# Kernel tuning notes

Hardware: AMD Instinct MI355X
Metric: run time of the kernel (lower is better)

Reference implementation:

```python
import jax, jax.numpy as jnp
import numpy as np

B, T, D, H, C = 32, 512, 768, 512, 7


def setup_inputs() -> dict:
    key = jax.random.key(0)
    ks = jax.random.split(key, 10)
    g = lambda k, shape: jax.random.normal(k, shape, jnp.float32) * 0.02
    return {
        "x": jax.random.normal(ks[0], (B, T, D), jnp.float32),
        # PyTorch LSTM params; b = b_ih + b_hh folded into one bias (same math)
        "Wf_ih": g(ks[1], (4 * H, 2 * D)),
        "Wf_hh": g(ks[2], (4 * H, H)),
        "bf": jnp.zeros((4 * H,), jnp.float32),
        "Wb_ih": g(ks[3], (4 * H, 2 * D)),
        "Wb_hh": g(ks[4], (4 * H, H)),
        "bb": jnp.zeros((4 * H,), jnp.float32),
        "W_enc": g(ks[5], (H, D)),
        "b_enc": jnp.zeros((H,), jnp.float32),
        "W_dec": g(ks[6], (H, H)),
        "b_dec": jnp.zeros((H,), jnp.float32),
        "v": jax.random.uniform(ks[7], (H,), jnpp := jnp.float32) if False else jax.random.uniform(ks[7], (H,), jnp.float32),
        "W_head": g(ks[8], (C, 2 * H)),
        "b_head": jnp.zeros((C,), jnp.float32),
    }


def reference(x, Wf_ih, Wf_hh, bf, Wb_ih, Wb_hh, bb, W_enc, b_enc, W_dec, b_dec, v, W_head, b_head):
    hid = W_dec.shape[0]
    # encoder projection is time-invariant -> hoist out of the loop (same math as original)
    enc_proj = jnp.einsum('btd,hd->bth', x, W_enc) + b_enc  # (B,T,H)

    def run_direction(x_seq, Wih, Whh, b):
        def step(carry, xt):
            h, c = carry                                    # (B,H) each
            dec = h @ W_dec.T + b_dec                       # (B,H)
            scores = jnp.tanh(enc_proj + dec[:, None, :]) @ v  # (B,T)
            w = jax.nn.softmax(scores, axis=1)
            ctx = jnp.einsum('bt,btd->bd', w, x)            # (B,D)
            inp = jnp.concatenate([ctx, xt], axis=1)        # (B,2D)
            gates = inp @ Wih.T + h @ Whh.T + b             # (B,4H), torch order i,f,g,o
            i_, f_, g_, o_ = jnp.split(gates, 4, axis=1)
            c = jax.nn.sigmoid(f_) * c + jax.nn.sigmoid(i_) * jnp.tanh(g_)
            h = jax.nn.sigmoid(o_) * jnp.tanh(c)
            return (h, c), h

        h0 = jnp.zeros((x.shape[0], hid), x.dtype)
        (_, _), hs = jax.lax.scan(step, (h0, h0), x_seq)
        return hs                                           # (T,B,H)

    x_seq = jnp.swapaxes(x, 0, 1)                           # (T,B,D)
    hs_f = run_direction(x_seq, Wf_ih, Wf_hh, bf)
    hs_b = run_direction(x_seq[::-1], Wb_ih, Wb_hh, bb)[::-1]
    comb = jnp.swapaxes(jnp.concatenate([hs_f, hs_b], axis=-1), 0, 1)  # (B,T,2H)
    return comb @ W_head.T + b_head                          # (B,T,C)
```

## Files before the change

### kernel.cpp

```cpp
#include <hip/hip_runtime.h>
#include <cstdint>
#include <cstddef>

#define L2E 1.4426950408889634f

typedef __attribute__((ext_vector_type(8))) short short8v;
typedef __attribute__((ext_vector_type(4))) float f32x4;
typedef unsigned long long ull;

__device__ __forceinline__ float fexp2(float x){ return __builtin_amdgcn_exp2f(x); }
__device__ __forceinline__ float frcp(float x){ return __builtin_amdgcn_rcpf(x); }
__device__ __forceinline__ float tanh_f(float x){
  return 1.f - 2.f*frcp(1.f + fexp2(2.f*L2E*x));
}
__device__ __forceinline__ float sigm_f(float x){
  return frcp(1.f + fexp2(-L2E*x));
}
__device__ __forceinline__ float bf2f(ushort u){ return __uint_as_float(((uint32_t)u)<<16); }
__device__ __forceinline__ ushort f2bf(float f){
  uint32_t x = __float_as_uint(f);
  uint32_t r = (x + 0x7FFFu + ((x>>16)&1u)) >> 16;
  return (ushort)r;
}

__device__ __forceinline__ float ld4f(const float* p){
  return __hip_atomic_load((float*)p, __ATOMIC_RELAXED, __HIP_MEMORY_SCOPE_AGENT);
}
__device__ __forceinline__ void st4f(float* p, float v){
  __hip_atomic_store(p, v, __ATOMIC_RELAXED, __HIP_MEMORY_SCOPE_AGENT);
}
__device__ __forceinline__ void st2h(ushort* p, ushort v){
  __hip_atomic_store(p, v, __ATOMIC_RELAXED, __HIP_MEMORY_SCOPE_AGENT);
}
__device__ __forceinline__ short8v ld16h(const ushort* p){
  union { ull u[2]; short8v s; } c;
  c.u[0] = __hip_atomic_load((ull*)p,     __ATOMIC_RELAXED, __HIP_MEMORY_SCOPE_AGENT);
  c.u[1] = __hip_atomic_load((ull*)(p+4), __ATOMIC_RELAXED, __HIP_MEMORY_SCOPE_AGENT);
  return c.s;
}
__device__ __forceinline__ void st8u(ushort* p, ull v){
  __hip_atomic_store((ull*)p, v, __ATOMIC_RELAXED, __HIP_MEMORY_SCOPE_AGENT);
}

namespace {
constexpr int NB = 32, TT = 512, DD = 768, HH = 512;
constexpr size_t EPB  = 0;
constexpr size_t XBB  = EPB  + (size_t)NB*HH*TT*2;
constexpr size_t HSB  = XBB  + (size_t)NB*TT*DD*2;
constexpr size_t WPKB = HSB  + (size_t)2*TT*NB*HH*2;
constexpr size_t WDPB = WPKB + (size_t)2*128*64*64*8*2;
constexpr size_t CTXB = WDPB + (size_t)32*16*64*8*2;
constexpr size_t CSTB = CTXB + (size_t)2*NB*DD*4;
constexpr size_t GSYB = CSTB + (size_t)2*NB*HH*4;
constexpr size_t WS_BYTES = GSYB + 32768;

constexpr int EPL  = 0;
constexpr int WPL  = 65536;
constexpr int REDL = 131072;
constexpr int HEVL = 147456;
constexpr int HBL  = 151680;
constexpr int DPL  = 153856;
constexpr int DECL = 155904;
constexpr int VVL  = 156416;
constexpr int CSCL = 156672;
constexpr int GFNL = 159776;
constexpr int LDS_BYTES = GFNL + 2176;
}

__device__ __forceinline__ void bar_arrive(uint* flags, uint token, int bid){
  __syncthreads();
  if (threadIdx.x == 0)
    __hip_atomic_store(&flags[bid*16], token, __ATOMIC_RELAXED, __HIP_MEMORY_SCOPE_AGENT);
}
__device__ __forceinline__ void bar_wait(uint* flags, uint token){
  if (threadIdx.x < 256) {
    while (__hip_atomic_load(&flags[threadIdx.x*16], __ATOMIC_RELAXED, __HIP_MEMORY_SCOPE_AGENT) < token)
      __builtin_amdgcn_s_sleep(1);
  }
  __syncthreads();
  asm volatile("" ::: "memory");
}

__global__ void k_xcast(const float* __restrict__ x, ushort* __restrict__ xb)
{
  size_t i = ((size_t)blockIdx.x*256 + threadIdx.x)*8;
  float4 v0 = *(const float4*)(x + i);
  float4 v1 = *(const float4*)(x + i + 4);
  short8v o;
  o[0]=(short)f2bf(v0.x); o[1]=(short)f2bf(v0.y); o[2]=(short)f2bf(v0.z); o[3]=(short)f2bf(v0.w);
  o[4]=(short)f2bf(v1.x); o[5]=(short)f2bf(v1.y); o[6]=(short)f2bf(v1.z); o[7]=(short)f2bf(v1.w);
  *(short8v*)(xb + i) = o;
}

__global__ void k_encproj(const float* __restrict__ x, const float* __restrict__ Wenc,
                          const float* __restrict__ benc, ushort* __restrict__ epT)
{
  int b = blockIdx.z, h0 = blockIdx.y*64, t0 = blockIdx.x*64;
  __shared__ float As[64][33];
  __shared__ float Bs[64][33];
  int tid = threadIdx.x;
  int n = tid & 63, mg = tid >> 6;
  float acc[16];
  #pragma unroll
  for (int j = 0; j < 16; j++) acc[j] = 0.f;
  int lr = tid >> 2, lk = (tid & 3) * 8;
  for (int k0 = 0; k0 < 768; k0 += 32) {
    const float* ap = Wenc + (size_t)(h0 + lr)*768 + k0 + lk;
    #pragma unroll
    for (int i = 0; i < 8; i++) As[lr][lk + i] = ap[i];
    const float* bp = x + ((size_t)b*512 + t0 + lr)*768 + k0 + lk;
    #pragma unroll
    for (int i = 0; i < 8; i++) Bs[lr][lk + i] = bp[i];
    __syncthreads();
    #pragma unroll
    for (int kk = 0; kk < 32; kk++) {
      float bv = Bs[n][kk];
      #pragma unroll
      for (int j = 0; j < 16; j++) acc[j] += As[mg*16 + j][kk] * bv;
    }
    __syncthreads();
  }
  #pragma unroll
  for (int j = 0; j < 16; j++) {
    int h = h0 + mg*16 + j;
    epT[((size_t)b*512 + h)*512 + t0 + n] = f2bf(acc[j] + benc[h]);
  }
}

__global__ void k_wpack(const float* __restrict__ Wfih, const float* __restrict__ Wfhh,
                        const float* __restrict__ Wbih, const float* __restrict__ Wbhh,
                        ushort* __restrict__ wpk)
{
  size_t f = (size_t)blockIdx.x*256 + threadIdx.x;
  int lane = (int)(f & 63), kstep = (int)((f>>6)&63), jblk = (int)((f>>12)&127), dir = (int)(f>>19);
  const float* Whh = dir ? Wbhh : Wfhh;
  const float* Wih = dir ? Wbih : Wfih;
  int c = lane & 15, gate = c >> 2, jj = c & 3;
  int row = gate*512 + jblk*4 + jj;
  int kbase = kstep*32 + (lane>>4)*8;
  short8v o;
  #pragma unroll
  for (int i = 0; i < 8; i++) {
    int k = kbase + i;
    float w = (k < 512) ? Whh[(size_t)row*512 + k] : Wih[(size_t)row*1536 + (k - 512)];
    o[i] = (short)f2bf(w);
  }
  *(short8v*)(wpk + f*8) = o;
}

__global__ void k_wdpack(const float* __restrict__ Wdec, ushort* __restrict__ wdp)
{
  int f = blockIdx.x*256 + threadIdx.x;
  int lane = f & 63, kstep = (f >> 6) & 15, nb = f >> 10;
  int n = nb*16 + (lane & 15);
  int kbase = kstep*32 + (lane >> 4)*8;
  short8v o;
  #pragma unroll
  for (int i = 0; i < 8; i++) o[i] = (short)f2bf(Wdec[(size_t)n*512 + kbase + i]);
  *(short8v*)(wdp + (size_t)f*8) = o;
}

__device__ __forceinline__ void gates_h(int s, int wid, int lane, int l15, int lk8, int dirG,
    const ushort* __restrict__ hsb, const ushort* wpk_l, float* RED)
{
  if (wid >= 2) return;
  int b0 = l15, b1 = 16 + l15;
  f32x4 acc0 = {0,0,0,0}, acc1 = {0,0,0,0};
  if (s > 0) {
    int t_prev = dirG ? (512 - s) : (s - 1);
    const ushort* h0 = hsb + (((size_t)dirG*512 + t_prev)*32 + b0)*512;
    const ushort* h1 = hsb + (((size_t)dirG*512 + t_prev)*32 + b1)*512;
    #pragma unroll
    for (int kk = 0; kk < 8; kk++) {
      int kstep = wid*8 + kk;
      int ko = kstep*32 + lk8;
      short8v a0v = *(const short8v*)(h0 + ko);
      short8v a1v = *(const short8v*)(h1 + ko);
      short8v bv  = *(const short8v*)(wpk_l + (size_t)kstep*512 + lane*8);
      acc0 = __builtin_amdgcn_mfma_f32_16x16x32_bf16(a0v, bv, acc0, 0, 0, 0);
      acc1 = __builtin_amdgcn_mfma_f32_16x16x32_bf16(a1v, bv, acc1, 0, 0, 0);
    }
  }
  int rr = (lane >> 4) * 4;
  #pragma unroll
  for (int r = 0; r < 4; r++) RED[((size_t)wid*32 + rr + r)*16 + l15] = acc0[r];
  #pragma unroll
  for (int r = 0; r < 4; r++) RED[((size_t)wid*32 + 16 + rr + r)*16 + l15] = acc1[r];
}

__device__ __forceinline__ void gates_x(int s, int wid, int lane, int l15, int lk8, int dirG,
    const ushort* __restrict__ xb, const ushort* wpk_l, float* RED)
{
  if (wid < 5) return;
  int b0 = l15, b1 = 16 + l15;
  f32x4 acc0 = {0,0,0,0}, acc1 = {0,0,0,0};
  int t_in = dirG ? (511 - s) : s;
  const ushort* x0 = xb + ((size_t)b0*512 + t_in)*768;
  const ushort* x1 = xb + ((size_t)b1*512 + t_in)*768;
  #pragma unroll
  for (int kk = 0; kk < 8; kk++) {
    int kstep = wid*8 + kk;
    int ko = kstep*32 - 1280 + lk8;
    short8v a0v = *(const short8v*)(x0 + ko);
    short8v a1v = *(const short8v*)(x1 + ko);
    short8v bv  = *(const short8v*)(wpk_l + (size_t)kstep*512 + lane*8);
    acc0 = __builtin_amdgcn_mfma_f32_16x16x32_bf16(a0v, bv, acc0, 0, 0, 0);
    acc1 = __builtin_amdgcn_mfma_f32_16x16x32_bf16(a1v, bv, acc1, 0, 0, 0);
  }
  int rr = (lane >> 4) * 4;
  #pragma unroll
  for (int r = 0; r < 4; r++) RED[((size_t)wid*32 + rr + r)*16 + l15] = acc0[r];
  #pragma unroll
  for (int r = 0; r < 4; r++) RED[((size_t)wid*32 + 16 + rr + r)*16 + l15] = acc1[r];
}

__global__ __launch_bounds__(512, 1) void k_loop(
    ushort* __restrict__ hsb, const ushort* __restrict__ xb, const ushort* __restrict__ ep,
    const ushort* __restrict__ wpk, const ushort* __restrict__ wdp,
    float* __restrict__ spart, ushort* __restrict__ ctxf,
    float* __restrict__ cst, const float* __restrict__ bdec, const float* __restrict__ vg,
    const float* __restrict__ bfv, const float* __restrict__ bbv,
    uint* __restrict__ flags, uint* __restrict__ gfl)
{
  extern __shared__ __align__(16) char dsm[];
  ushort* ep_l  = (ushort*)(dsm + EPL);
  ushort* wpk_l = (ushort*)(dsm + WPL);
  float*  RED   = (float*)(dsm + REDL);
  float*  HEV   = (float*)(dsm + HEVL);
  ushort* HB    = (ushort*)(dsm + HBL);
  float*  DP    = (float*)(dsm + DPL);
  float*  DEC   = (float*)(dsm + DECL);
  float*  VV    = (float*)(dsm + VVL);
  float*  CSC   = (float*)(dsm + CSCL);
  float*  GFIN  = (float*)(dsm + GFNL);

  const int bid = blockIdx.x;
  const int tid = threadIdx.x;
  const int wid = tid >> 6, lane = tid & 63;
  const int l15 = lane & 15, lk8 = (lane >> 4) * 8;
  const int bS = bid >> 3, hc = bid & 7;
  const int dirG = bid >> 7, jblkG = bid & 127;
  uint bar_t = 0;

  {
    const short8v* esrc = (const short8v*)(ep + ((size_t)bS*512 + hc*64)*512);
    short8v* edst = (short8v*)ep_l;
    for (int i = tid; i < 4096; i += 512) edst[i] = esrc[i];
    const short8v* wsrc = (const short8v*)(wpk + (((size_t)dirG*128 + jblkG)*64)*512);
    short8v* wdst = (short8v*)wpk_l;
    for (int i = tid; i < 4096; i += 512) wdst[i] = wsrc[i];
    if (tid < 64) VV[tid] = vg[hc*64 + tid];
  }
  ++bar_t; bar_arrive(flags, bar_t, bid);
  gates_x(0, wid, lane, l15, lk8, dirG, xb, wpk_l, RED);
  bar_wait(flags, bar_t);

  for (int s = 0; s < TT; ++s) {
    if (s == 0) {
      if (tid < 128) { int dir = tid >> 6, n = tid & 63; DEC[dir*64 + n] = bdec[hc*64 + n]; }
    } else {
      if (tid < 128) {
        int dir = tid >> 6, q = tid & 63;
        int tp = dir ? (512 - s) : (s - 1);
        short8v hv = *(const short8v*)(hsb + (((size_t)dir*512 + tp)*32 + bS)*512 + q*8);
        *(short8v*)&HB[(dir*4 + (q >> 4))*136 + (q & 15)*8] = hv;
      }
      __syncthreads();
      {
        int dir = tid >> 8, n = (tid >> 2) & 63, kq = tid & 3;
        int ng = hc*64 + n, nb = ng >> 4, c = ng & 15;
        const ushort* hrow = HB + (dir*4 + kq)*136;
        float a = 0.f;
        #pragma unroll
        for (int ch = 0; ch < 16; ch++) {
          int kstep = kq*4 + (ch >> 2), lhi = ch & 3;
          short8v w8 = *(const short8v*)(wdp + (((size_t)nb*16 + kstep)*64 + lhi*16 + c)*8);
          #pragma unroll
          for (int j = 0; j < 8; j++) a += bf2f((ushort)w8[j]) * bf2f(hrow[ch*8 + j]);
        }
        DP[tid] = a;
      }
      __syncthreads();
      if (tid < 128) {
        int dir = tid >> 6, n = tid & 63;
        const float* dp = DP + dir*256 + n*4;
        DEC[dir*64 + n] = dp[0] + dp[1] + dp[2] + dp[3] + bdec[hc*64 + n];
      }
    }
    __syncthreads();

    float s0 = 0.f, s1 = 0.f;
    {
      int t = tid;
      #pragma unroll 8
      for (int h = 0; h < 64; h++) {
        float e = bf2f(ep_l[h*512 + t]);
        float vv = VV[h];
        s0 += tanh_f(e + DEC[h]) * vv;
        s1 += tanh_f(e + DEC[64 + h]) * vv;
      }
    }

    {
      float* sp = spart + (((size_t)(bS*8 + hc))*2)*512;
      st4f(sp + tid, s0);
      st4f(sp + 512 + tid, s1);
      __syncthreads();
      if (tid == 0)
        __hip_atomic_store(&gfl[bid*16], (uint)(s + 1), __ATOMIC_RELAXED, __HIP_MEMORY_SCOPE_AGENT);
      gates_h(s, wid, lane, l15, lk8, dirG, hsb, wpk_l, RED);
      if (tid >= 128 && tid < 136) {
        while (__hip_atomic_load(&gfl[(bS*8 + (tid - 128))*16], __ATOMIC_RELAXED, __HIP_MEMORY_SCOPE_AGENT) < (uint)(s + 1))
          __builtin_amdgcn_s_sleep(1);
      }
      __syncthreads();
      float s0r = 0.f, s1r = 0.f;
      #pragma unroll
      for (int j = 0; j < 8; j++) {
        const float* spj = spart + (((size_t)(bS*8 + j))*2)*512;
        s0r += ld4f(spj + tid);
        s1r += ld4f(spj + 512 + tid);
      }
      s0r = fminf(s0r, 100.f); s1r = fminf(s1r, 100.f);
      float e0 = fexp2((s0r - 32.f)*L2E);
      float e1 = fexp2((s1r - 32.f)*L2E);
      float z0 = e0, z1 = e1;
      #pragma unroll
      for (int off = 32; off; off >>= 1) { z0 += __shfl_xor(z0, off); z1 += __shfl_xor(z1, off); }
      if (lane == 0) { DP[wid] = z0; DP[8 + wid] = z1; }
      __syncthreads();
      if (tid < 2) {
        float z = 0.f;
        #pragma unroll
        for (int w = 0; w < 8; w++) z += DP[tid*8 + w];
        DP[128 + tid] = frcp(z);
      }
      __syncthreads();
      e0 *= DP[128]; e1 *= DP[129];
      HEV[(tid >> 7)*132 + (tid & 127)] = e0;
      HEV[(4 + (tid >> 7))*132 + (tid & 127)] = e1;
      __syncthreads();
    }

    if (tid < 384) {
      int dl = tid % 96, tq = tid / 96;
      const ushort* xp = xb + (((size_t)bS*512 + tq*128)*768) + hc*96 + dl;
      const float* ev0 = HEV + tq*132;
      const float* ev1 = HEV + (4 + tq)*132;
      float a0 = 0.f, a1 = 0.f;
      #pragma unroll 8
      for (int t2 = 0; t2 < 128; t2++) {
        float xv = bf2f(xp[(size_t)t2*768]);
        a0 += ev0[t2]*xv;
        a1 += ev1[t2]*xv;
      }
      CSC[(tq*2 + 0)*97 + dl] = a0;
      CSC[(tq*2 + 1)*97 + dl] = a1;
    }
    __syncthreads();
    if (tid < 192) {
      int dl = tid % 96, dir = tid / 96;
      float cv = CSC[(0*2 + dir)*97 + dl] + CSC[(1*2 + dir)*97 + dl]
               + CSC[(2*2 + dir)*97 + dl] + CSC[(3*2 + dir)*97 + dl];
      st2h(ctxf + ((size_t)dir*32 + bS)*768 + hc*96 + dl, f2bf(cv));
    }

    ++bar_t; bar_arrive(flags, bar_t, bid);
    bar_wait(flags, bar_t);

    {
      if (wid >= 2 && wid <= 4) {
        int b0 = l15, b1 = 16 + l15;
        f32x4 acc0 = {0,0,0,0}, acc1 = {0,0,0,0};
        const ushort* c0 = ctxf + ((size_t)dirG*32 + b0)*768;
        const ushort* c1 = ctxf + ((size_t)dirG*32 + b1)*768;
        #pragma unroll
        for (int kk = 0; kk < 8; kk++) {
          int kstep = wid*8 + kk;
          int ko = kstep*32 - 512 + lk8;
          short8v a0v = ld16h(c0 + ko);
          short8v a1v = ld16h(c1 + ko);
          short8v bv  = *(const short8v*)(wpk_l + (size_t)kstep*512 + lane*8);
          acc0 = __builtin_amdgcn_mfma_f32_16x16x32_bf16(a0v, bv, acc0, 0, 0, 0);
          acc1 = __builtin_amdgcn_mfma_f32_16x16x32_bf16(a1v, bv, acc1, 0, 0, 0);
        }
        int rr = (lane >> 4) * 4;
        #pragma unroll
        for (int r = 0; r < 4; r++) RED[((size_t)wid*32 + rr + r)*16 + l15] = acc0[r];
        #pragma unroll
        for (int r = 0; r < 4; r++) RED[((size_t)wid*32 + 16 + rr + r)*16 + l15] = acc1[r];
      }
      __syncthreads();
      {
        int bb = tid >> 4, c = tid & 15;
        float g = 0.f;
        #pragma unroll
        for (int w = 0; w < 8; w++) g += RED[((size_t)w*32 + bb)*16 + c];
        GFIN[bb*17 + c] = g;
      }
      __syncthreads();
      if (tid < 32) {
        int b = tid;
        int j0 = jblkG*4;
        const float* bias = dirG ? bbv : bfv;
        size_t ci0 = ((size_t)dirG*32 + b)*512 + j0;
        float4 co = *(const float4*)&cst[ci0];
        float cold[4] = {co.x, co.y, co.z, co.w};
        float4 cn4;
        ull hp = 0;
        #pragma unroll
        for (int jj = 0; jj < 4; jj++) {
          int j = j0 + jj;
          float gi  = GFIN[b*17 + jj]       + bias[j];
          float gf  = GFIN[b*17 + 4 + jj]   + bias[512 + j];
          float gg  = GFIN[b*17 + 8 + jj]   + bias[1024 + j];
          float go_ = GFIN[b*17 + 12 + jj]  + bias[1536 + j];
          float cn = sigm_f(gf)*cold[jj] + sigm_f(gi)*tanh_f(gg);
          float h  = sigm_f(go_)*tanh_f(cn);
          ((float*)&cn4)[jj] = cn;
          hp |= ((ull)f2bf(h)) << (16*jj);
        }
        *(float4*)&cst[ci0] = cn4;
        int tw = dirG ? (511 - s) : s;
        st8u(hsb + (((size_t)dirG*512 + tw)*32 + b)*512 + j0, hp);
      }
    }
    ++bar_t; bar_arrive(flags, bar_t, bid);
    if (s + 1 < TT)
      gates_x(s + 1, wid, lane, l15, lk8, dirG, xb, wpk_l, RED);
    bar_wait(flags, bar_t);
  }
}

__global__ void k_head(const ushort* __restrict__ hsb, const float* __restrict__ Wh,
                       const float* __restrict__ bh, float* __restrict__ out)
{
  int wid = threadIdx.x >> 6, lane = threadIdx.x & 63;
  int r = blockIdx.x*4 + wid;
  int b = r >> 9, t = r & 511;
  float acc[7];
  #pragma unroll
  for (int c = 0; c < 7; c++) acc[c] = 0.f;
  const ushort* hf = hsb + (((size_t)t)*32 + b)*512;
  const ushort* hb = hsb + (((size_t)512 + t)*32 + b)*512;
  for (int k0 = 0; k0 < 512; k0 += 64) {
    int k = k0 + lane;
    float a = bf2f(hf[k]), bvv = bf2f(hb[k]);
    #pragma unroll
    for (int c = 0; c < 7; c++)
      acc[c] += a*Wh[c*1024 + k] + bvv*Wh[c*1024 + 512 + k];
  }
  #pragma unroll
  for (int c = 0; c < 7; c++) {
    float sres = acc[c];
    #pragma unroll
    for (int off = 32; off; off >>= 1) sres += __shfl_xor(sres, off);
    if (lane == c) out[((size_t)b*512 + t)*7 + c] = sres + bh[c];
  }
}

extern "C" void kernel_launch(void* const* d_in, const int* in_sizes, int n_in,
                              void* d_out, int out_size, void* d_ws, size_t ws_size,
                              hipStream_t stream) {
  (void)in_sizes; (void)n_in; (void)out_size;
  const float* x    = (const float*)d_in[0];
  const float* Wfih = (const float*)d_in[1];
  const float* Wfhh = (const float*)d_in[2];
  const float* bfv  = (const float*)d_in[3];
  const float* Wbih = (const float*)d_in[4];
  const float* Wbhh = (const float*)d_in[5];
  const float* bbv  = (const float*)d_in[6];
  const float* Wenc = (const float*)d_in[7];
  const float* benc = (const float*)d_in[8];
  const float* Wdec = (const float*)d_in[9];
  const float* bdec = (const float*)d_in[10];
  const float* v    = (const float*)d_in[11];
  const float* Whead= (const float*)d_in[12];
  const float* bhead= (const float*)d_in[13];
  float* out = (float*)d_out;
  char* ws = (char*)d_ws;

  if (ws_size < WS_BYTES) return;

  ushort* ep   = (ushort*)(ws + EPB);
  float*  spart= (float*)(ws + EPB);
  ushort* xb   = (ushort*)(ws + XBB);
  ushort* hsb  = (ushort*)(ws + HSB);
  ushort* wpk  = (ushort*)(ws + WPKB);
  ushort* wdp  = (ushort*)(ws + WDPB);
  ushort* ctxf = (ushort*)(ws + CTXB);
  float*  cst  = (float*)(ws + CSTB);
  uint*   flags= (uint*)(ws + GSYB);
  uint*   gfl  = (uint*)(ws + GSYB + 16384);

  hipFuncSetAttribute(reinterpret_cast<const void*>(k_loop),
                      hipFuncAttributeMaxDynamicSharedMemorySize, LDS_BYTES);

  hipMemsetAsync(ws + CSTB, 0, (size_t)2*NB*HH*4, stream);
  hipMemsetAsync(ws + GSYB, 0, 32768, stream);

  hipLaunchKernelGGL(k_xcast, dim3(6144), dim3(256), 0, stream, x, xb);
  hipLaunchKernelGGL(k_encproj, dim3(8,8,32), dim3(256), 0, stream, x, Wenc, benc, ep);
  hipLaunchKernelGGL(k_wpack, dim3(4096), dim3(256), 0, stream, Wfih, Wfhh, Wbih, Wbhh, wpk);
  hipLaunchKernelGGL(k_wdpack, dim3(128), dim3(256), 0, stream, Wdec, wdp);

  void* args[] = {
    (void*)&hsb, (void*)&xb, (void*)&ep, (void*)&wpk, (void*)&wdp,
    (void*)&spart, (void*)&ctxf, (void*)&cst,
    (void*)&bdec, (void*)&v, (void*)&bfv, (void*)&bbv,
    (void*)&flags, (void*)&gfl
  };
  hipLaunchCooperativeKernel(reinterpret_cast<void*>(k_loop), dim3(256), dim3(512),
                             args, LDS_BYTES, stream);

  hipLaunchKernelGGL(k_head, dim3(4096), dim3(256), 0, stream, hsb, Whead, bhead, out);
}
```

Before: 14.87 ms.

## Replace all-to-all score exchange with tagged-value reduction at leader block

Per-step attention score partials are now written as 64-bit words that carry a step tag alongside the value. The leader block (hc==0) of each batch polls for and sums the partials, computes the softmax weights and publishes them tagged; the other blocks poll for those weights instead of each reading all eight partials. This removes the per-block flag stores, flag spins and the extra __syncthreads, and the leader defers its gates_h work until after the barrier arrive. The cost is word-level spin polling on global memory and a serialised dependency on the leader block.

```diff
diff --git a/kernel.cpp b/kernel.cpp
--- a/kernel.cpp
+++ b/kernel.cpp
@@ -40,6 +40,12 @@
 }
 __device__ __forceinline__ void st8u(ushort* p, ull v){
   __hip_atomic_store((ull*)p, v, __ATOMIC_RELAXED, __HIP_MEMORY_SCOPE_AGENT);
+}
+__device__ __forceinline__ ull ld8a(const ull* p){
+  return __hip_atomic_load((ull*)p, __ATOMIC_RELAXED, __HIP_MEMORY_SCOPE_AGENT);
+}
+__device__ __forceinline__ void st8a(ull* p, ull v){
+  __hip_atomic_store(p, v, __ATOMIC_RELAXED, __HIP_MEMORY_SCOPE_AGENT);
 }
 
 namespace {
@@ -50,9 +56,10 @@
 constexpr size_t WPKB = HSB  + (size_t)2*TT*NB*HH*2;
 constexpr size_t WDPB = WPKB + (size_t)2*128*64*64*8*2;
 constexpr size_t CTXB = WDPB + (size_t)32*16*64*8*2;
-constexpr size_t CSTB = CTXB + (size_t)2*NB*DD*4;
+constexpr size_t EVGB = CTXB + (size_t)2*NB*DD*4;
+constexpr size_t CSTB = EVGB + (size_t)NB*2*512*8;
 constexpr size_t GSYB = CSTB + (size_t)2*NB*HH*4;
-constexpr size_t WS_BYTES = GSYB + 32768;
+constexpr size_t WS_BYTES = GSYB + 49152;
 
 constexpr int EPL  = 0;
 constexpr int WPL  = 65536;
@@ -217,10 +224,10 @@
 __global__ __launch_bounds__(512, 1) void k_loop(
     ushort* __restrict__ hsb, const ushort* __restrict__ xb, const ushort* __restrict__ ep,
     const ushort* __restrict__ wpk, const ushort* __restrict__ wdp,
-    float* __restrict__ spart, ushort* __restrict__ ctxf,
+    ull* __restrict__ spart_u, ushort* __restrict__ ctxf, ull* __restrict__ evt_u,
     float* __restrict__ cst, const float* __restrict__ bdec, const float* __restrict__ vg,
     const float* __restrict__ bfv, const float* __restrict__ bbv,
-    uint* __restrict__ flags, uint* __restrict__ gfl)
+    uint* __restrict__ flags)
 {
   extern __shared__ __align__(16) char dsm[];
   ushort* ep_l  = (ushort*)(dsm + EPL);
@@ -256,6 +263,8 @@
   bar_wait(flags, bar_t);
 
   for (int s = 0; s < TT; ++s) {
+    const uint want = 0xA0000000u | (uint)(s + 1);
+
     if (s == 0) {
       if (tid < 128) { int dir = tid >> 6, n = tid & 63; DEC[dir*64 + n] = bdec[hc*64 + n]; }
     } else {
@@ -301,26 +310,58 @@
       }
     }
 
-    {
-      float* sp = spart + (((size_t)(bS*8 + hc))*2)*512;
-      st4f(sp + tid, s0);
-      st4f(sp + 512 + tid, s1);
-      __syncthreads();
-      if (tid == 0)
-        __hip_atomic_store(&gfl[bid*16], (uint)(s + 1), __ATOMIC_RELAXED, __HIP_MEMORY_SCOPE_AGENT);
+    if (hc != 0) {
+      ull hi = ((ull)want) << 32;
+      st8a(spart_u + (((size_t)(bS*8 + hc))*2 + 0)*512 + tid, hi | (ull)__float_as_uint(s0));
+      st8a(spart_u + (((size_t)(bS*8 + hc))*2 + 1)*512 + tid, hi | (ull)__float_as_uint(s1));
       gates_h(s, wid, lane, l15, lk8, dirG, hsb, wpk_l, RED);
-      if (tid >= 128 && tid < 136) {
-        while (__hip_atomic_load(&gfl[(bS*8 + (tid - 128))*16], __ATOMIC_RELAXED, __HIP_MEMORY_SCOPE_AGENT) < (uint)(s + 1))
-          __builtin_amdgcn_s_sleep(1);
-      }
-      __syncthreads();
-      float s0r = 0.f, s1r = 0.f;
-      #pragma unroll
-      for (int j = 0; j < 8; j++) {
-        const float* spj = spart + (((size_t)(bS*8 + j))*2)*512;
-        s0r += ld4f(spj + tid);
-        s1r += ld4f(spj + 512 + tid);
-      }
+      float e0 = 0.f, e1 = 0.f;
+      {
+        uint pend = 3u;
+        while (pend) {
+          if (pend & 1u) {
+            ull u = ld8a(evt_u + ((size_t)bS*2 + 0)*512 + tid);
+            if ((uint)(u >> 32) == want) { e0 = __uint_as_float((uint)u); pend &= ~1u; }
+          }
+          if (pend & 2u) {
+            ull u = ld8a(evt_u + ((size_t)bS*2 + 1)*512 + tid);
+            if ((uint)(u >> 32) == want) { e1 = __uint_as_float((uint)u); pend &= ~2u; }
+          }
+          if (pend) __builtin_amdgcn_s_sleep(1);
+        }
+      }
+      HEV[(tid >> 7)*132 + (tid & 127)] = e0;
+      HEV[(4 + (tid >> 7))*132 + (tid & 127)] = e1;
+      __syncthreads();
+    } else {
+      float v0,v1,v2,v3,v4,v5,v6,v7,v8,v9,v10,v11,v12,v13;
+      v0=v1=v2=v3=v4=v5=v6=v7=v8=v9=v10=v11=v12=v13=0.f;
+      {
+        uint pend = 0x3FFFu;
+        while (pend) {
+          #pragma unroll
+          for (int k = 0; k < 14; k++) {
+            if (pend & (1u << k)) {
+              int j = (k >> 1) + 1, dir = k & 1;
+              ull u = ld8a(spart_u + (((size_t)(bS*8 + j))*2 + dir)*512 + tid);
+              if ((uint)(u >> 32) == want) {
+                float f = __uint_as_float((uint)u);
+                switch (k) {
+                  case 0: v0=f; break; case 1: v1=f; break; case 2: v2=f; break;
+                  case 3: v3=f; break; case 4: v4=f; break; case 5: v5=f; break;
+                  case 6: v6=f; break; case 7: v7=f; break; case 8: v8=f; break;
+                  case 9: v9=f; break; case 10: v10=f; break; case 11: v11=f; break;
+                  case 12: v12=f; break; default: v13=f; break;
+                }
+                pend &= ~(1u << k);
+              }
+            }
+          }
+          if (pend) __builtin_amdgcn_s_sleep(1);
+        }
+      }
+      float s0r = s0 + v0 + v2 + v4 + v6 + v8 + v10 + v12;
+      float s1r = s1 + v1 + v3 + v5 + v7 + v9 + v11 + v13;
       s0r = fminf(s0r, 100.f); s1r = fminf(s1r, 100.f);
       float e0 = fexp2((s0r - 32.f)*L2E);
       float e1 = fexp2((s1r - 32.f)*L2E);
@@ -337,6 +378,9 @@
       }
       __syncthreads();
       e0 *= DP[128]; e1 *= DP[129];
+      ull hi = ((ull)want) << 32;
+      st8a(evt_u + ((size_t)bS*2 + 0)*512 + tid, hi | (ull)__float_as_uint(e0));
+      st8a(evt_u + ((size_t)bS*2 + 1)*512 + tid, hi | (ull)__float_as_uint(e1));
       HEV[(tid >> 7)*132 + (tid & 127)] = e0;
       HEV[(4 + (tid >> 7))*132 + (tid & 127)] = e1;
       __syncthreads();
@@ -366,6 +410,7 @@
     }
 
     ++bar_t; bar_arrive(flags, bar_t, bid);
+    if (hc == 0) gates_h(s, wid, lane, l15, lk8, dirG, hsb, wpk_l, RED);
     bar_wait(flags, bar_t);
 
     {
@@ -483,21 +528,22 @@
   if (ws_size < WS_BYTES) return;
 
   ushort* ep   = (ushort*)(ws + EPB);
-  float*  spart= (float*)(ws + EPB);
+  ull*    spart= (ull*)(ws + EPB);
   ushort* xb   = (ushort*)(ws + XBB);
   ushort* hsb  = (ushort*)(ws + HSB);
   ushort* wpk  = (ushort*)(ws + WPKB);
   ushort* wdp  = (ushort*)(ws + WDPB);
   ushort* ctxf = (ushort*)(ws + CTXB);
+  ull*    evtu = (ull*)(ws + EVGB);
   float*  cst  = (float*)(ws + CSTB);
   uint*   flags= (uint*)(ws + GSYB);
-  uint*   gfl  = (uint*)(ws + GSYB + 16384);
 
   hipFuncSetAttribute(reinterpret_cast<const void*>(k_loop),
                       hipFuncAttributeMaxDynamicSharedMemorySize, LDS_BYTES);
 
   hipMemsetAsync(ws + CSTB, 0, (size_t)2*NB*HH*4, stream);
-  hipMemsetAsync(ws + GSYB, 0, 32768, stream);
+  hipMemsetAsync(ws + GSYB, 0, 49152, stream);
+  hipMemsetAsync(ws + EVGB, 0, (size_t)NB*2*512*8, stream);
 
   hipLaunchKernelGGL(k_xcast, dim3(6144), dim3(256), 0, stream, x, xb);
   hipLaunchKernelGGL(k_encproj, dim3(8,8,32), dim3(256), 0, stream, x, Wenc, benc, ep);
@@ -506,9 +552,9 @@
 
   void* args[] = {
     (void*)&hsb, (void*)&xb, (void*)&ep, (void*)&wpk, (void*)&wdp,
-    (void*)&spart, (void*)&ctxf, (void*)&cst,
+    (void*)&spart, (void*)&ctxf, (void*)&evtu, (void*)&cst,
     (void*)&bdec, (void*)&v, (void*)&bfv, (void*)&bbv,
-    (void*)&flags, (void*)&gfl
+    (void*)&flags
   };
   hipLaunchCooperativeKernel(reinterpret_cast<void*>(k_loop), dim3(256), dim3(512),
                              args, LDS_BYTES, stream);
```

New measurement: 16.63 ms. 11.8% more time.
